# Optimization experiments

Hardware: AMD Instinct MI355X
Metric: run time of the kernel (lower is better)

## Reference

```python
import jax, jax.numpy as jnp
import numpy as np

BN_EPS = 1e-5
NUM_BITS = 8          # activation quantization bits
NUM_BITS_WEIGHT = 8   # weight quantization bits


def _ste(x, q):
    # straight-through estimator: forward = q, backward = identity
    return x + jax.lax.stop_gradient(q - x)


def quant_signed(x, bits):
    # symmetric signed per-tensor uniform quantization (input_signed=True / weights with sign=True)
    qmax = float(2 ** (bits - 1) - 1)
    scale = jnp.max(jnp.abs(x)) / qmax + 1e-12
    q = jnp.clip(jnp.round(x / scale), -qmax - 1.0, qmax) * scale
    return _ste(x, q)


def quant_unsigned(x, bits):
    # unsigned per-tensor uniform quantization (input_signed=False, post-ReLU activations)
    qmax = float(2 ** bits - 1)
    scale = jnp.max(x) / qmax + 1e-12
    q = jnp.clip(jnp.round(x / scale), 0.0, qmax) * scale
    return _ste(x, q)


def conv3x3(x, w, stride=1):
    # x: [N,C,H,W], w: [O,I,3,3], padding=1, no bias
    return jax.lax.conv_general_dilated(
        x, w, window_strides=(stride, stride), padding=((1, 1), (1, 1)),
        dimension_numbers=('NCHW', 'OIHW', 'NCHW'))


def batchnorm(x, gamma, beta):
    # training-mode BN: per-batch statistics over (N,H,W)
    mean = jnp.mean(x, axis=(0, 2, 3), keepdims=True)
    var = jnp.var(x, axis=(0, 2, 3), keepdims=True)
    xn = (x - mean) * jax.lax.rsqrt(var + BN_EPS)
    return xn * gamma[None, :, None, None] + beta[None, :, None, None]


def setup_inputs() -> dict:
    key = jax.random.key(0)
    k1, k2, k3 = jax.random.split(key, 3)
    B, C, H, W = 64, 256, 32, 32
    x = jax.random.normal(k1, (B, C, H, W), dtype=jnp.float32)
    fan = C * 9
    w1 = jax.random.normal(k2, (C, C, 3, 3), dtype=jnp.float32) * np.sqrt(2.0 / fan)
    w2 = jax.random.normal(k3, (C, C, 3, 3), dtype=jnp.float32) * np.sqrt(2.0 / fan)
    gamma1 = jnp.ones((C,), jnp.float32)
    beta1 = jnp.zeros((C,), jnp.float32)
    gamma2 = jnp.ones((C,), jnp.float32)
    beta2 = jnp.zeros((C,), jnp.float32)
    return {'x': x, 'w1': w1, 'gamma1': gamma1, 'beta1': beta1,
            'w2': w2, 'gamma2': gamma2, 'beta2': beta2}


def reference(x, w1, gamma1, beta1, w2, gamma2, beta2):
    residual = x
    # conv1: input_signed=True -> signed 8-bit act quant; weight 8-bit signed quant
    qx = quant_signed(x, NUM_BITS)
    qw1 = quant_signed(w1, NUM_BITS_WEIGHT)
    out = conv3x3(qx, qw1, stride=1)
    out = batchnorm(out, gamma1, beta1)
    out = jax.nn.relu(out)
    # conv2: input_signed=False -> unsigned 8-bit act quant (post-ReLU)
    qo = quant_unsigned(out, NUM_BITS)
    qw2 = quant_signed(w2, NUM_BITS_WEIGHT)
    out = conv3x3(qo, qw2, stride=1)
    out = batchnorm(out, gamma2, beta2)
    out = out + residual
    out = jax.nn.relu(out)
    return out
```

## Files before the change

kernel.cpp:

```cpp
#include <hip/hip_runtime.h>

typedef __attribute__((ext_vector_type(4))) int i32x4;

typedef __attribute__((address_space(1))) unsigned int uglobal;
typedef __attribute__((address_space(3))) unsigned int ulocal;

__device__ __forceinline__ void async16(const void* g, void* l) {
  __builtin_amdgcn_global_load_lds((const uglobal*)g, (ulocal*)l, 16, 0, 0);
}
__device__ __forceinline__ float u2f(unsigned u) { return __uint_as_float(u); }

__global__ __launch_bounds__(256) void absmax3_kernel(const float* __restrict__ x,
                                                      const float* __restrict__ w1,
                                                      const float* __restrict__ w2,
                                                      unsigned* __restrict__ sc) {
  int b = blockIdx.x;
  const float* src; int n4, b0, nb, seg;
  if (b < 1792)      { src = x;  n4 = 4194304; b0 = 0;    nb = 1792; seg = 0; }
  else if (b < 1856) { src = w1; n4 = 147456;  b0 = 1792; nb = 64;   seg = 1; }
  else               { src = w2; n4 = 147456;  b0 = 1856; nb = 64;   seg = 2; }
  float m = 0.f;
  int stride = nb * 256;
  for (int i = (b - b0) * 256 + threadIdx.x; i < n4; i += stride) {
    float4 v = ((const float4*)src)[i];
    m = fmaxf(fmaxf(fabsf(v.x), fabsf(v.y)), fmaxf(fmaxf(fabsf(v.z), fabsf(v.w)), m));
  }
  for (int off = 32; off; off >>= 1) m = fmaxf(m, __shfl_down(m, off, 64));
  __shared__ float sm[4];
  int lane = threadIdx.x & 63, wv = threadIdx.x >> 6;
  if (!lane) sm[wv] = m;
  __syncthreads();
  if (threadIdx.x == 0)
    atomicMax(sc + seg, __float_as_uint(fmaxf(fmaxf(sm[0], sm[1]), fmaxf(sm[2], sm[3]))));
}

__global__ __launch_bounds__(256) void quantw_kernel(const float* __restrict__ w1,
                                                     const float* __restrict__ w2,
                                                     signed char* __restrict__ wq1,
                                                     signed char* __restrict__ wq2,
                                                     const unsigned* __restrict__ sc,
                                                     int* __restrict__ csumT) {
  int b = blockIdx.x, which = b >> 8, o = b & 255, t = threadIdx.x;
  const float* w = which ? w2 : w1;
  signed char* wq = which ? wq2 : wq1;
  float s = u2f(sc[1 + which]) / 127.f + 1e-12f;
  __shared__ float lw[2304];
  for (int j = t; j < 2304; j += 256) lw[j] = w[(size_t)o * 2304 + j];
  __syncthreads();
  int ssum = 0;
#pragma unroll
  for (int tap = 0; tap < 9; ++tap) {
    float q = fminf(fmaxf(rintf(lw[t * 9 + tap] / s), -128.f), 127.f);
    wq[(size_t)o * 2304 + tap * 256 + t] = (signed char)q;
    ssum += (int)q;
  }
  if (which) {
    for (int off = 32; off; off >>= 1) ssum += __shfl_down(ssum, off, 64);
    __shared__ int si[4];
    if (!(t & 63)) si[t >> 6] = ssum;
    __syncthreads();
    if (t == 0) csumT[o] = 128 * (si[0] + si[1] + si[2] + si[3]);
  }
}

__global__ __launch_bounds__(256) void border_kernel(signed char* __restrict__ halo, int v) {
  int n = blockIdx.x;
  int4 val = make_int4(v, v, v, v);
  for (int it = 0; it < 9; ++it) {
    int slot = it * 256 + threadIdx.x;
    if (slot >= 2112) break;
    int cell = slot >> 4, sub = slot & 15;
    int h, w;
    if (cell < 34)      { h = 0;  w = cell; }
    else if (cell < 68) { h = 33; w = cell - 34; }
    else { int j = cell - 68; h = 1 + (j >> 1); w = (j & 1) * 33; }
    *(int4*)(halo + ((size_t)((n * 34 + h) * 34) + w) * 256 + sub * 16) = val;
  }
}

__global__ __launch_bounds__(256) void quantx_kernel(const float* __restrict__ x,
                                                     signed char* __restrict__ halo,
                                                     const unsigned* __restrict__ sc) {
  int n = blockIdx.x >> 5, h = blockIdx.x & 31;
  float s = u2f(sc[0]) / 127.f + 1e-12f;
  __shared__ float lds[32 * 257];
  const float* src = x + (size_t)n * 262144 + h * 32;
  int t = threadIdx.x;
  int wloc = t & 31, crow = t >> 5;
  for (int cc = 0; cc < 256; cc += 8) {
    int c = cc + crow;
    lds[wloc * 257 + c] = src[(size_t)c * 1024 + wloc];
  }
  __syncthreads();
  signed char* dst = halo + ((size_t)((n * 34 + h + 1) * 34) + 1) * 256;
  int c4 = (t & 63) * 4, wsub = t >> 6;
  for (int j = 0; j < 8; ++j) {
    int w_ = wsub * 8 + j;
    char4 q;
    q.x = (signed char)fminf(fmaxf(rintf(lds[w_ * 257 + c4 + 0] / s), -128.f), 127.f);
    q.y = (signed char)fminf(fmaxf(rintf(lds[w_ * 257 + c4 + 1] / s), -128.f), 127.f);
    q.z = (signed char)fminf(fmaxf(rintf(lds[w_ * 257 + c4 + 2] / s), -128.f), 127.f);
    q.w = (signed char)fminf(fmaxf(rintf(lds[w_ * 257 + c4 + 3] / s), -128.f), 127.f);
    *(char4*)(dst + (size_t)w_ * 256 + c4) = q;
  }
}

template <int MODE>
__global__ __launch_bounds__(512) void conv_i8_kernel(const signed char* __restrict__ aptr,
                                                      const signed char* __restrict__ bptr,
                                                      float* __restrict__ out,
                                                      const unsigned* __restrict__ sc,
                                                      float* __restrict__ part,
                                                      const int* __restrict__ csumT) {
  extern __shared__ char smem[];
  const int tid = threadIdx.x, lane = tid & 63, wid = tid >> 6;
  const int wm = wid >> 2, wn = wid & 3;
  int bid = blockIdx.x;
  bid = (bid & 7) * 32 + (bid >> 3);
  const int pixBase = bid * 256;

  long gA[2], gB[2];
  int ldst[2];
#pragma unroll
  for (int j = 0; j < 2; ++j) {
    int d = tid * 16 + j * 8192;
    int rp = d >> 7, s5 = (d >> 4) & 7, sp = s5 ^ (rp & 7);
    int row = rp * 2 + (sp >> 2), kc = (sp & 3) * 16;
    ldst[j] = d;
    int p = pixBase + row;
    int n = p >> 10, h = (p >> 5) & 31, w_ = p & 31;
    long ghalo = (long)((n * 34 + h) * 34 + w_) * 256 + kc;
    long gwt = (long)row * 2304 + kc;
    gA[j] = (MODE == 0) ? ghalo : gwt;
    gB[j] = (MODE == 0) ? gwt : ghalo;
  }

  const int g = lane >> 4, l15 = lane & 15;
  int aOff[8], bOff[4];
#pragma unroll
  for (int m = 0; m < 8; ++m) {
    int row = wm * 128 + m * 16 + l15; int rp = row >> 1;
    aOff[m] = rp * 128 + (((((row & 1) << 2) | g) ^ (rp & 7)) << 4);
  }
#pragma unroll
  for (int n = 0; n < 4; ++n) {
    int row = wn * 64 + n * 16 + l15; int rp = row >> 1;
    bOff[n] = rp * 128 + (((((row & 1) << 2) | g) ^ (rp & 7)) << 4);
  }

  const char* ac = (const char*)aptr;
  const char* bc = (const char*)bptr;
  char* lds = smem;

  auto stageH = [&](int P, int h) {
    int cblk = P / 9, tap = P - cblk * 9;
    int kh = tap / 3, kw = tap - kh * 3;
    long uH = (long)(kh * 34 + kw) * 256 + cblk * 64;
    long uW = (long)tap * 256 + cblk * 64;
    char* rb = lds + (P & 3) * 32768;
    if (h == 0) {
      long uA = (MODE == 0) ? uH : uW;
      async16(ac + gA[0] + uA, rb + ldst[0]);
      async16(ac + gA[1] + uA, rb + ldst[1]);
    } else {
      long uB = (MODE == 0) ? uW : uH;
      async16(bc + gB[0] + uB, rb + 16384 + ldst[0]);
      async16(bc + gB[1] + uB, rb + 16384 + ldst[1]);
    }
  };

  i32x4 acc[8][4];
#pragma unroll
  for (int m = 0; m < 8; ++m)
#pragma unroll
    for (int n = 0; n < 4; ++n)
#pragma unroll
      for (int r = 0; r < 4; ++r) acc[m][n][r] = 0;

  stageH(0, 0); stageH(0, 1); stageH(1, 0); stageH(1, 1); stageH(2, 0); stageH(2, 1);
  asm volatile("s_waitcnt vmcnt(8)" ::: "memory");
  __builtin_amdgcn_s_barrier();

  for (int P = 0; P < 36; ++P) {
    const char* rb = lds + (P & 3) * 32768;
    i32x4 a[8], b[4];
#pragma unroll
    for (int m = 0; m < 4; ++m) a[m] = *(const i32x4*)(rb + aOff[m]);
#pragma unroll
    for (int n = 0; n < 4; ++n) b[n] = *(const i32x4*)(rb + 16384 + bOff[n]);
    if (P < 33) stageH(P + 3, 0);
    __builtin_amdgcn_s_barrier();
    asm volatile("s_waitcnt lgkmcnt(0)" ::: "memory");
    __builtin_amdgcn_sched_barrier(0);
    __builtin_amdgcn_s_setprio(1);
#pragma unroll
    for (int m = 0; m < 4; ++m)
#pragma unroll
      for (int n = 0; n < 4; ++n)
        acc[m][n] = __builtin_amdgcn_mfma_i32_16x16x64_i8(a[m], b[n], acc[m][n], 0, 0, 0);
    __builtin_amdgcn_s_setprio(0);
    __builtin_amdgcn_s_barrier();
#pragma unroll
    for (int m = 4; m < 8; ++m) a[m] = *(const i32x4*)(rb + aOff[m]);
    if (P < 33) stageH(P + 3, 1);
    __builtin_amdgcn_s_barrier();
    asm volatile("s_waitcnt lgkmcnt(0)" ::: "memory");
    __builtin_amdgcn_sched_barrier(0);
    __builtin_amdgcn_s_setprio(1);
#pragma unroll
    for (int m = 4; m < 8; ++m)
#pragma unroll
      for (int n = 0; n < 4; ++n)
        acc[m][n] = __builtin_amdgcn_mfma_i32_16x16x64_i8(a[m], b[n], acc[m][n], 0, 0, 0);
    __builtin_amdgcn_s_setprio(0);
    if (P < 33)       asm volatile("s_waitcnt vmcnt(8)" ::: "memory");
    else if (P == 33) asm volatile("s_waitcnt vmcnt(4)" ::: "memory");
    else if (P == 34) asm volatile("s_waitcnt vmcnt(0)" ::: "memory");
    if (P < 35) __builtin_amdgcn_s_barrier();
  }
  __syncthreads();

  float* twr = (float*)(smem + wid * 17408);

  if constexpr (MODE == 0) {
    const float s = (u2f(sc[0]) / 127.f + 1e-12f) * (u2f(sc[1]) / 127.f + 1e-12f);
    float vs[4], vss[4], vmx[4], vmn[4];
#pragma unroll
    for (int n = 0; n < 4; ++n) { vs[n] = 0.f; vss[n] = 0.f; vmx[n] = -3.4e38f; vmn[n] = 3.4e38f; }
#pragma unroll
    for (int half = 0; half < 2; ++half) {
#pragma unroll
      for (int m2 = 0; m2 < 4; ++m2) {
        int m = half * 4 + m2;
#pragma unroll
        for (int n = 0; n < 4; ++n)
#pragma unroll
          for (int r = 0; r < 4; ++r) {
            float v = (float)acc[m][n][r] * s;
            vs[n] += v; vss[n] += v * v;
            vmx[n] = fmaxf(vmx[n], v); vmn[n] = fminf(vmn[n], v);
            twr[(m2 * 16 + g * 4 + r) * 68 + n * 16 + l15] = v;
          }
      }
#pragma unroll
      for (int it = 0; it < 16; ++it) {
        int i = it * 64 + lane;
        int row = i >> 4, c4 = (i & 15) << 2;
        float4 v4 = *(const float4*)(twr + row * 68 + c4);
        int p = pixBase + wm * 128 + half * 64 + row;
        *(float4*)(out + (size_t)p * 256 + wn * 64 + c4) = v4;
      }
    }
#pragma unroll
    for (int off = 16; off <= 32; off <<= 1)
#pragma unroll
      for (int n = 0; n < 4; ++n) {
        vs[n] += __shfl_xor(vs[n], off, 64);
        vss[n] += __shfl_xor(vss[n], off, 64);
        vmx[n] = fmaxf(vmx[n], __shfl_xor(vmx[n], off, 64));
        vmn[n] = fminf(vmn[n], __shfl_xor(vmn[n], off, 64));
      }
    __syncthreads();
    float* S0 = (float*)(smem + 139264);
    float* S1 = S0 + 512; float* S2 = S0 + 1024; float* S3 = S0 + 1536;
    if (lane < 16) {
#pragma unroll
      for (int n = 0; n < 4; ++n) {
        int ch = wn * 64 + n * 16 + l15;
        S0[wm * 256 + ch] = vs[n]; S1[wm * 256 + ch] = vss[n];
        S2[wm * 256 + ch] = vmx[n]; S3[wm * 256 + ch] = vmn[n];
      }
    }
    __syncthreads();
    if (tid < 256) {
      int idx = bid * 256 + tid;
      part[idx]          = S0[tid] + S0[256 + tid];
      part[65536 + idx]  = S1[tid] + S1[256 + tid];
      part[131072 + idx] = fmaxf(S2[tid], S2[256 + tid]);
      part[196608 + idx] = fminf(S3[tid], S3[256 + tid]);
    }
  } else {
    const float s = (u2f(sc[3]) / 255.f + 1e-12f) * (u2f(sc[2]) / 127.f + 1e-12f);
    float* SS = (float*)(smem + 139264);
    float* SQ = SS + 1024;
#pragma unroll
    for (int half = 0; half < 2; ++half) {
#pragma unroll
      for (int m2 = 0; m2 < 4; ++m2) {
        int m = half * 4 + m2;
        int o0 = wm * 128 + half * 64 + m2 * 16 + g * 4;
        i32x4 tc = *(const i32x4*)(csumT + o0);
        float sr[4] = {0.f, 0.f, 0.f, 0.f}, sq[4] = {0.f, 0.f, 0.f, 0.f};
#pragma unroll
        for (int n = 0; n < 4; ++n)
#pragma unroll
          for (int r = 0; r < 4; ++r) {
            float v = (float)(acc[m][n][r] + tc[r]) * s;
            sr[r] += v; sq[r] += v * v;
            twr[(m2 * 16 + g * 4 + r) * 68 + n * 16 + l15] = v;
          }
#pragma unroll
        for (int off = 1; off <= 8; off <<= 1)
#pragma unroll
          for (int r = 0; r < 4; ++r) {
            sr[r] += __shfl_xor(sr[r], off, 64);
            sq[r] += __shfl_xor(sq[r], off, 64);
          }
        if (l15 == 0) {
#pragma unroll
          for (int r = 0; r < 4; ++r) {
            SS[wn * 256 + o0 + r] = sr[r];
            SQ[wn * 256 + o0 + r] = sq[r];
          }
        }
      }
#pragma unroll
      for (int it = 0; it < 16; ++it) {
        int i = it * 64 + lane;
        int row = i >> 4, c4 = (i & 15) << 2;
        float4 v4 = *(const float4*)(twr + row * 68 + c4);
        int o = wm * 128 + half * 64 + row;
        *(float4*)(out + (size_t)o * 65536 + pixBase + wn * 64 + c4) = v4;
      }
    }
    __syncthreads();
    if (tid < 256) {
      float a = 0.f, b = 0.f;
#pragma unroll
      for (int w = 0; w < 4; ++w) { a += SS[w * 256 + tid]; b += SQ[w * 256 + tid]; }
      part[bid * 256 + tid] = a;
      part[65536 + bid * 256 + tid] = b;
    }
  }
}

__global__ __launch_bounds__(256) void bn1fin_kernel(const float* __restrict__ part,
                                                     const float* __restrict__ g,
                                                     const float* __restrict__ be,
                                                     float* __restrict__ bnA, float* __restrict__ bnB,
                                                     unsigned* __restrict__ sc) {
  int o0 = blockIdx.x * 32;
  int t = threadIdx.x, oc = t & 31, mq = t >> 5;
  float s = 0.f, ss = 0.f, mx = -3.4e38f, mn = 3.4e38f;
  for (int j = 0; j < 32; ++j) {
    int i = (mq * 32 + j) * 256 + o0 + oc;
    s += part[i]; ss += part[65536 + i];
    mx = fmaxf(mx, part[131072 + i]); mn = fminf(mn, part[196608 + i]);
  }
  __shared__ float red[4][8][32];
  red[0][mq][oc] = s; red[1][mq][oc] = ss; red[2][mq][oc] = mx; red[3][mq][oc] = mn;
  __syncthreads();
  if (t < 32) {
    s = 0.f; ss = 0.f; mx = -3.4e38f; mn = 3.4e38f;
    for (int q = 0; q < 8; ++q) {
      s += red[0][q][t]; ss += red[1][q][t];
      mx = fmaxf(mx, red[2][q][t]); mn = fminf(mn, red[3][q][t]);
    }
    float mean = s * (1.f / 65536.f);
    float var = fmaxf(ss * (1.f / 65536.f) - mean * mean, 0.f);
    int o = o0 + t;
    float a = g[o] * rsqrtf(var + 1e-5f);
    float b2 = be[o] - mean * a;
    bnA[o] = a; bnB[o] = b2;
    float m = fmaxf(fmaxf(a * mx + b2, a * mn + b2), 0.f);
    atomicMax(sc + 3, __float_as_uint(m));
  }
}

__global__ __launch_bounds__(256) void bn2fin_kernel(const float* __restrict__ part,
                                                     const float* __restrict__ g,
                                                     const float* __restrict__ be,
                                                     float* __restrict__ bnA2, float* __restrict__ bnB2) {
  int o0 = blockIdx.x * 32;
  int t = threadIdx.x, oc = t & 31, mq = t >> 5;
  float s = 0.f, ss = 0.f;
  for (int j = 0; j < 32; ++j) {
    int i = (mq * 32 + j) * 256 + o0 + oc;
    s += part[i]; ss += part[65536 + i];
  }
  __shared__ float red[2][8][32];
  red[0][mq][oc] = s; red[1][mq][oc] = ss;
  __syncthreads();
  if (t < 32) {
    s = 0.f; ss = 0.f;
    for (int q = 0; q < 8; ++q) { s += red[0][q][t]; ss += red[1][q][t]; }
    float mean = s * (1.f / 65536.f);
    float var = fmaxf(ss * (1.f / 65536.f) - mean * mean, 0.f);
    int o = o0 + t;
    float a = g[o] * rsqrtf(var + 1e-5f);
    bnA2[o] = a;
    bnB2[o] = be[o] - mean * a;
  }
}

__global__ __launch_bounds__(256) void apply_kernel(const float* __restrict__ y,
                                                    const float* __restrict__ bnA,
                                                    const float* __restrict__ bnB,
                                                    const unsigned* __restrict__ sc,
                                                    signed char* __restrict__ halo) {
  int t = threadIdx.x;
  int c4 = (t & 63) * 4;
  int psub = t >> 6;
  float s2 = u2f(sc[3]) / 255.f + 1e-12f;
  float4 a = *(const float4*)(bnA + c4);
  float4 b = *(const float4*)(bnB + c4);
  int p0 = blockIdx.x * 16 + psub;
  for (int j = 0; j < 4; ++j) {
    int p = p0 + j * 4;
    float4 v = *(const float4*)(y + (size_t)p * 256 + c4);
    char4 q;
    q.x = (signed char)((int)fminf(fmaxf(rintf(fmaxf(a.x * v.x + b.x, 0.f) / s2), 0.f), 255.f) - 128);
    q.y = (signed char)((int)fminf(fmaxf(rintf(fmaxf(a.y * v.y + b.y, 0.f) / s2), 0.f), 255.f) - 128);
    q.z = (signed char)((int)fminf(fmaxf(rintf(fmaxf(a.z * v.z + b.z, 0.f) / s2), 0.f), 255.f) - 128);
    q.w = (signed char)((int)fminf(fmaxf(rintf(fmaxf(a.w * v.w + b.w, 0.f) / s2), 0.f), 255.f) - 128);
    int n = p >> 10, h = (p >> 5) & 31, w_ = p & 31;
    *(char4*)(halo + ((size_t)((n * 34 + h + 1) * 34) + (w_ + 1)) * 256 + c4) = q;
  }
}

__global__ __launch_bounds__(256) void final_kernel(const float* __restrict__ y2,
                                                    const float* __restrict__ x,
                                                    const float* __restrict__ bnA2,
                                                    const float* __restrict__ bnB2,
                                                    float* __restrict__ out) {
  int tid = blockIdx.x * 256 + threadIdx.x;
  for (int i = tid; i < 4194304; i += 1048576) {
    int e = i << 2;
    int o = (e >> 10) & 255;
    int n = e >> 18, hw = e & 1023;
    float4 v = *(const float4*)(y2 + (((size_t)o << 16) + (n << 10) + hw));
    float4 xr = ((const float4*)x)[i];
    float a = bnA2[o], b = bnB2[o];
    float4 r;
    r.x = fmaxf(a * v.x + b + xr.x, 0.f);
    r.y = fmaxf(a * v.y + b + xr.y, 0.f);
    r.z = fmaxf(a * v.z + b + xr.z, 0.f);
    r.w = fmaxf(a * v.w + b + xr.w, 0.f);
    ((float4*)out)[i] = r;
  }
}

extern "C" void kernel_launch(void* const* d_in, const int* in_sizes, int n_in,
                              void* d_out, int out_size, void* d_ws, size_t ws_size,
                              hipStream_t stream) {
  const float* x  = (const float*)d_in[0];
  const float* w1 = (const float*)d_in[1];
  const float* g1 = (const float*)d_in[2];
  const float* b1 = (const float*)d_in[3];
  const float* w2 = (const float*)d_in[4];
  const float* g2 = (const float*)d_in[5];
  const float* b2 = (const float*)d_in[6];
  float* out = (float*)d_out;
  char* ws = (char*)d_ws;

  unsigned* sc = (unsigned*)ws;
  float* bnA   = (float*)(ws + 4096);
  float* bnB   = (float*)(ws + 8192);
  float* bnA2  = (float*)(ws + 12288);
  float* bnB2  = (float*)(ws + 16384);
  int*   csumT = (int*)(ws + 20480);
  float* part  = (float*)(ws + 24576);
  signed char* wq1  = (signed char*)(ws + 24576 + 1048576);
  signed char* wq2  = wq1 + 589824;
  signed char* halo = wq2 + 589824;
  float* convb = (float*)(ws + 24576 + 1048576 + 2 * 589824 + 18939904);

  hipFuncSetAttribute((const void*)(conv_i8_kernel<0>), hipFuncAttributeMaxDynamicSharedMemorySize, 147456);
  hipFuncSetAttribute((const void*)(conv_i8_kernel<1>), hipFuncAttributeMaxDynamicSharedMemorySize, 147456);

  hipMemsetAsync(sc, 0, 64, stream);
  border_kernel<<<64, 256, 0, stream>>>(halo, 0);

  absmax3_kernel<<<1920, 256, 0, stream>>>(x, w1, w2, sc);
  quantw_kernel<<<512, 256, 0, stream>>>(w1, w2, wq1, wq2, sc, csumT);
  quantx_kernel<<<2048, 256, 0, stream>>>(x, halo, sc);
  conv_i8_kernel<0><<<256, 512, 147456, stream>>>(halo, wq1, convb, sc, part, csumT);
  bn1fin_kernel<<<8, 256, 0, stream>>>(part, g1, b1, bnA, bnB, sc);
  border_kernel<<<64, 256, 0, stream>>>(halo, (int)0x80808080u);
  apply_kernel<<<4096, 256, 0, stream>>>(convb, bnA, bnB, sc, halo);
  conv_i8_kernel<1><<<256, 512, 147456, stream>>>(wq2, halo, convb, sc, part, csumT);
  bn2fin_kernel<<<8, 256, 0, stream>>>(part, g2, b2, bnA2, bnB2);
  final_kernel<<<4096, 256, 0, stream>>>(convb, x, bnA2, bnB2, out);
}
```

Measured before the change: 315.8 us.

## Fuse BN stats, finalize and apply into conv epilogues via grid barrier

The BN finalize, apply/quantize and final residual kernels are folded into the conv kernels. Per-channel statistics are combined with global atomics (float add plus order-preserving keys for max/min), followed by a software grid-wide barrier, after which each block applies BN in registers and writes either quantized int8 into a second halo buffer or the final output. This removes the fp32 intermediate conv buffer round-trips and several launches. It also simplifies the main loop to a single barrier stage per step, and it relies on all 256 blocks being co-resident for the spin barrier, which risks deadlock and adds atomic contention.

```diff
diff --git a/kernel.cpp b/kernel.cpp
--- a/kernel.cpp
+++ b/kernel.cpp
@@ -9,6 +9,26 @@
   __builtin_amdgcn_global_load_lds((const uglobal*)g, (ulocal*)l, 16, 0, 0);
 }
 __device__ __forceinline__ float u2f(unsigned u) { return __uint_as_float(u); }
+
+__device__ __forceinline__ unsigned fkey(float f) {
+  unsigned u = __float_as_uint(f);
+  return u ^ (unsigned)(((int)u >> 31) | (int)0x80000000);
+}
+__device__ __forceinline__ float funkey(unsigned k) {
+  unsigned u = (k & 0x80000000u) ? (k ^ 0x80000000u) : ~k;
+  return __uint_as_float(u);
+}
+
+__device__ __forceinline__ void gridbar(unsigned* ctr) {
+  __syncthreads();
+  if (threadIdx.x == 0) {
+    __threadfence();
+    atomicAdd(ctr, 1u);
+    while (atomicAdd(ctr, 0u) < 256u) __builtin_amdgcn_s_sleep(2);
+    __threadfence();
+  }
+  __syncthreads();
+}
 
 __global__ __launch_bounds__(256) void absmax3_kernel(const float* __restrict__ x,
                                                       const float* __restrict__ w1,
@@ -63,8 +83,11 @@
   }
 }
 
-__global__ __launch_bounds__(256) void border_kernel(signed char* __restrict__ halo, int v) {
-  int n = blockIdx.x;
+__global__ __launch_bounds__(256) void border_kernel(signed char* __restrict__ h1,
+                                                     signed char* __restrict__ h2) {
+  int which = blockIdx.x >> 6, n = blockIdx.x & 63;
+  signed char* halo = which ? h2 : h1;
+  int v = which ? (int)0x80808080u : 0;
   int4 val = make_int4(v, v, v, v);
   for (int it = 0; it < 9; ++it) {
     int slot = it * 256 + threadIdx.x;
@@ -108,9 +131,13 @@
 template <int MODE>
 __global__ __launch_bounds__(512) void conv_i8_kernel(const signed char* __restrict__ aptr,
                                                       const signed char* __restrict__ bptr,
-                                                      float* __restrict__ out,
-                                                      const unsigned* __restrict__ sc,
-                                                      float* __restrict__ part,
+                                                      const float* __restrict__ xres,
+                                                      float* __restrict__ outp,
+                                                      signed char* __restrict__ halo2,
+                                                      const float* __restrict__ gam,
+                                                      const float* __restrict__ bet,
+                                                      unsigned* __restrict__ sc,
+                                                      float* __restrict__ red,
                                                       const int* __restrict__ csumT) {
   extern __shared__ char smem[];
   const int tid = threadIdx.x, lane = tid & 63, wid = tid >> 6;
@@ -152,21 +179,18 @@
   const char* bc = (const char*)bptr;
   char* lds = smem;
 
-  auto stageH = [&](int P, int h) {
+  auto stage = [&](int P) {
     int cblk = P / 9, tap = P - cblk * 9;
     int kh = tap / 3, kw = tap - kh * 3;
     long uH = (long)(kh * 34 + kw) * 256 + cblk * 64;
     long uW = (long)tap * 256 + cblk * 64;
+    long uA = (MODE == 0) ? uH : uW;
+    long uB = (MODE == 0) ? uW : uH;
     char* rb = lds + (P & 3) * 32768;
-    if (h == 0) {
-      long uA = (MODE == 0) ? uH : uW;
-      async16(ac + gA[0] + uA, rb + ldst[0]);
-      async16(ac + gA[1] + uA, rb + ldst[1]);
-    } else {
-      long uB = (MODE == 0) ? uW : uH;
-      async16(bc + gB[0] + uB, rb + 16384 + ldst[0]);
-      async16(bc + gB[1] + uB, rb + 16384 + ldst[1]);
-    }
+    async16(ac + gA[0] + uA, rb + ldst[0]);
+    async16(ac + gA[1] + uA, rb + ldst[1]);
+    async16(bc + gB[0] + uB, rb + 16384 + ldst[0]);
+    async16(bc + gB[1] + uB, rb + 16384 + ldst[1]);
   };
 
   i32x4 acc[8][4];
@@ -177,38 +201,21 @@
 #pragma unroll
       for (int r = 0; r < 4; ++r) acc[m][n][r] = 0;
 
-  stageH(0, 0); stageH(0, 1); stageH(1, 0); stageH(1, 1); stageH(2, 0); stageH(2, 1);
+  stage(0); stage(1); stage(2);
   asm volatile("s_waitcnt vmcnt(8)" ::: "memory");
-  __builtin_amdgcn_s_barrier();
+  asm volatile("s_barrier" ::: "memory");
 
   for (int P = 0; P < 36; ++P) {
+    if (P < 33) stage(P + 3);
     const char* rb = lds + (P & 3) * 32768;
     i32x4 a[8], b[4];
 #pragma unroll
-    for (int m = 0; m < 4; ++m) a[m] = *(const i32x4*)(rb + aOff[m]);
+    for (int m = 0; m < 8; ++m) a[m] = *(const i32x4*)(rb + aOff[m]);
 #pragma unroll
     for (int n = 0; n < 4; ++n) b[n] = *(const i32x4*)(rb + 16384 + bOff[n]);
-    if (P < 33) stageH(P + 3, 0);
-    __builtin_amdgcn_s_barrier();
-    asm volatile("s_waitcnt lgkmcnt(0)" ::: "memory");
-    __builtin_amdgcn_sched_barrier(0);
     __builtin_amdgcn_s_setprio(1);
 #pragma unroll
-    for (int m = 0; m < 4; ++m)
-#pragma unroll
-      for (int n = 0; n < 4; ++n)
-        acc[m][n] = __builtin_amdgcn_mfma_i32_16x16x64_i8(a[m], b[n], acc[m][n], 0, 0, 0);
-    __builtin_amdgcn_s_setprio(0);
-    __builtin_amdgcn_s_barrier();
-#pragma unroll
-    for (int m = 4; m < 8; ++m) a[m] = *(const i32x4*)(rb + aOff[m]);
-    if (P < 33) stageH(P + 3, 1);
-    __builtin_amdgcn_s_barrier();
-    asm volatile("s_waitcnt lgkmcnt(0)" ::: "memory");
-    __builtin_amdgcn_sched_barrier(0);
-    __builtin_amdgcn_s_setprio(1);
-#pragma unroll
-    for (int m = 4; m < 8; ++m)
+    for (int m = 0; m < 8; ++m)
 #pragma unroll
       for (int n = 0; n < 4; ++n)
         acc[m][n] = __builtin_amdgcn_mfma_i32_16x16x64_i8(a[m], b[n], acc[m][n], 0, 0, 0);
@@ -216,41 +223,27 @@
     if (P < 33)       asm volatile("s_waitcnt vmcnt(8)" ::: "memory");
     else if (P == 33) asm volatile("s_waitcnt vmcnt(4)" ::: "memory");
     else if (P == 34) asm volatile("s_waitcnt vmcnt(0)" ::: "memory");
-    if (P < 35) __builtin_amdgcn_s_barrier();
-  }
-  __syncthreads();
-
+    if (P < 35) asm volatile("s_barrier" ::: "memory");
+  }
+  __syncthreads();
+
+  unsigned* redu = (unsigned*)red;
   float* twr = (float*)(smem + wid * 17408);
 
   if constexpr (MODE == 0) {
-    const float s = (u2f(sc[0]) / 127.f + 1e-12f) * (u2f(sc[1]) / 127.f + 1e-12f);
     float vs[4], vss[4], vmx[4], vmn[4];
 #pragma unroll
     for (int n = 0; n < 4; ++n) { vs[n] = 0.f; vss[n] = 0.f; vmx[n] = -3.4e38f; vmn[n] = 3.4e38f; }
 #pragma unroll
-    for (int half = 0; half < 2; ++half) {
-#pragma unroll
-      for (int m2 = 0; m2 < 4; ++m2) {
-        int m = half * 4 + m2;
-#pragma unroll
-        for (int n = 0; n < 4; ++n)
-#pragma unroll
-          for (int r = 0; r < 4; ++r) {
-            float v = (float)acc[m][n][r] * s;
-            vs[n] += v; vss[n] += v * v;
-            vmx[n] = fmaxf(vmx[n], v); vmn[n] = fminf(vmn[n], v);
-            twr[(m2 * 16 + g * 4 + r) * 68 + n * 16 + l15] = v;
-          }
-      }
-#pragma unroll
-      for (int it = 0; it < 16; ++it) {
-        int i = it * 64 + lane;
-        int row = i >> 4, c4 = (i & 15) << 2;
-        float4 v4 = *(const float4*)(twr + row * 68 + c4);
-        int p = pixBase + wm * 128 + half * 64 + row;
-        *(float4*)(out + (size_t)p * 256 + wn * 64 + c4) = v4;
-      }
-    }
+    for (int m = 0; m < 8; ++m)
+#pragma unroll
+      for (int n = 0; n < 4; ++n)
+#pragma unroll
+        for (int r = 0; r < 4; ++r) {
+          float v = (float)acc[m][n][r];
+          vs[n] += v; vss[n] += v * v;
+          vmx[n] = fmaxf(vmx[n], v); vmn[n] = fminf(vmn[n], v);
+        }
 #pragma unroll
     for (int off = 16; off <= 32; off <<= 1)
 #pragma unroll
@@ -260,7 +253,6 @@
         vmx[n] = fmaxf(vmx[n], __shfl_xor(vmx[n], off, 64));
         vmn[n] = fminf(vmn[n], __shfl_xor(vmn[n], off, 64));
       }
-    __syncthreads();
     float* S0 = (float*)(smem + 139264);
     float* S1 = S0 + 512; float* S2 = S0 + 1024; float* S3 = S0 + 1536;
     if (lane < 16) {
@@ -273,170 +265,161 @@
     }
     __syncthreads();
     if (tid < 256) {
-      int idx = bid * 256 + tid;
-      part[idx]          = S0[tid] + S0[256 + tid];
-      part[65536 + idx]  = S1[tid] + S1[256 + tid];
-      part[131072 + idx] = fmaxf(S2[tid], S2[256 + tid]);
-      part[196608 + idx] = fminf(S3[tid], S3[256 + tid]);
+      atomicAdd(red + tid, S0[tid] + S0[256 + tid]);
+      atomicAdd(red + 256 + tid, S1[tid] + S1[256 + tid]);
+      atomicMax(redu + 512 + tid, fkey(fmaxf(S2[tid], S2[256 + tid])));
+      atomicMin(redu + 768 + tid, fkey(fminf(S3[tid], S3[256 + tid])));
+    }
+    gridbar(sc + 8);
+    float* bnAl = (float*)(smem + 139264);
+    float* bnBl = bnAl + 256;
+    float* rmx  = bnAl + 512;
+    const float sDq = (u2f(sc[0]) / 127.f + 1e-12f) * (u2f(sc[1]) / 127.f + 1e-12f);
+    if (tid < 256) {
+      float su  = atomicAdd(red + tid, 0.f);
+      float sq  = atomicAdd(red + 256 + tid, 0.f);
+      float mxr = funkey(atomicAdd(redu + 512 + tid, 0u));
+      float mnr = funkey(atomicAdd(redu + 768 + tid, 0u));
+      float mean = sDq * su * (1.f / 65536.f);
+      float e2 = sDq * sDq * sq * (1.f / 65536.f);
+      float var = fmaxf(e2 - mean * mean, 0.f);
+      float a = gam[tid] * rsqrtf(var + 1e-5f);
+      float b = bet[tid] - mean * a;
+      float aS = a * sDq;
+      bnAl[tid] = aS; bnBl[tid] = b;
+      rmx[tid] = fmaxf(fmaxf(aS * mxr + b, aS * mnr + b), 0.f);
+    }
+    __syncthreads();
+    for (int st = 128; st; st >>= 1) {
+      if (tid < st) rmx[tid] = fmaxf(rmx[tid], rmx[tid + st]);
+      __syncthreads();
+    }
+    float s2 = rmx[0] * (1.f / 255.f) + 1e-12f;
+    if (tid == 0) ((float*)sc)[3] = s2;
+    float is2 = 1.f / s2;
+    float aCh[4], bCh[4];
+#pragma unroll
+    for (int n = 0; n < 4; ++n) {
+      aCh[n] = bnAl[wn * 64 + n * 16 + l15];
+      bCh[n] = bnBl[wn * 64 + n * 16 + l15];
+    }
+#pragma unroll
+    for (int half = 0; half < 2; ++half) {
+#pragma unroll
+      for (int m2 = 0; m2 < 4; ++m2) {
+        int m = half * 4 + m2;
+#pragma unroll
+        for (int n = 0; n < 4; ++n)
+#pragma unroll
+          for (int r = 0; r < 4; ++r) {
+            float y = fmaxf(aCh[n] * (float)acc[m][n][r] + bCh[n], 0.f);
+            twr[(m2 * 16 + g * 4 + r) * 68 + n * 16 + l15] = y;
+          }
+      }
+#pragma unroll
+      for (int it = 0; it < 16; ++it) {
+        int i = it * 64 + lane;
+        int row = i >> 4, c4 = (i & 15) << 2;
+        float4 y4 = *(const float4*)(twr + row * 68 + c4);
+        char4 q;
+        q.x = (signed char)((int)fminf(fmaxf(rintf(y4.x * is2), 0.f), 255.f) - 128);
+        q.y = (signed char)((int)fminf(fmaxf(rintf(y4.y * is2), 0.f), 255.f) - 128);
+        q.z = (signed char)((int)fminf(fmaxf(rintf(y4.z * is2), 0.f), 255.f) - 128);
+        q.w = (signed char)((int)fminf(fmaxf(rintf(y4.w * is2), 0.f), 255.f) - 128);
+        int p = pixBase + wm * 128 + half * 64 + row;
+        int n_ = p >> 10, h = (p >> 5) & 31, w_ = p & 31;
+        *(char4*)(halo2 + ((size_t)((n_ * 34 + h + 1) * 34) + (w_ + 1)) * 256 + wn * 64 + c4) = q;
+      }
     }
   } else {
-    const float s = (u2f(sc[3]) / 255.f + 1e-12f) * (u2f(sc[2]) / 127.f + 1e-12f);
+    const float s2f = ((const float*)sc)[3];
+    const float sDq = s2f * (u2f(sc[2]) / 127.f + 1e-12f);
     float* SS = (float*)(smem + 139264);
     float* SQ = SS + 1024;
 #pragma unroll
-    for (int half = 0; half < 2; ++half) {
+    for (int half = 0; half < 2; ++half)
 #pragma unroll
       for (int m2 = 0; m2 < 4; ++m2) {
         int m = half * 4 + m2;
         int o0 = wm * 128 + half * 64 + m2 * 16 + g * 4;
         i32x4 tc = *(const i32x4*)(csumT + o0);
-        float sr[4] = {0.f, 0.f, 0.f, 0.f}, sq[4] = {0.f, 0.f, 0.f, 0.f};
+        float sr[4] = {0.f, 0.f, 0.f, 0.f}, sq_[4] = {0.f, 0.f, 0.f, 0.f};
 #pragma unroll
         for (int n = 0; n < 4; ++n)
 #pragma unroll
           for (int r = 0; r < 4; ++r) {
-            float v = (float)(acc[m][n][r] + tc[r]) * s;
-            sr[r] += v; sq[r] += v * v;
-            twr[(m2 * 16 + g * 4 + r) * 68 + n * 16 + l15] = v;
+            float vd = (float)(acc[m][n][r] + tc[r]);
+            sr[r] += vd; sq_[r] += vd * vd;
           }
 #pragma unroll
         for (int off = 1; off <= 8; off <<= 1)
 #pragma unroll
           for (int r = 0; r < 4; ++r) {
             sr[r] += __shfl_xor(sr[r], off, 64);
-            sq[r] += __shfl_xor(sq[r], off, 64);
+            sq_[r] += __shfl_xor(sq_[r], off, 64);
           }
         if (l15 == 0) {
 #pragma unroll
           for (int r = 0; r < 4; ++r) {
             SS[wn * 256 + o0 + r] = sr[r];
-            SQ[wn * 256 + o0 + r] = sq[r];
+            SQ[wn * 256 + o0 + r] = sq_[r];
           }
         }
+      }
+    __syncthreads();
+    if (tid < 256) {
+      float a_ = 0.f, b_ = 0.f;
+#pragma unroll
+      for (int w = 0; w < 4; ++w) { a_ += SS[w * 256 + tid]; b_ += SQ[w * 256 + tid]; }
+      atomicAdd(red + 1024 + tid, a_);
+      atomicAdd(red + 1280 + tid, b_);
+    }
+    gridbar(sc + 9);
+    float* a2l = (float*)(smem + 139264);
+    float* b2l = a2l + 256;
+    if (tid < 256) {
+      float su = atomicAdd(red + 1024 + tid, 0.f);
+      float sq = atomicAdd(red + 1280 + tid, 0.f);
+      float mean = sDq * su * (1.f / 65536.f);
+      float e2 = sDq * sDq * sq * (1.f / 65536.f);
+      float var = fmaxf(e2 - mean * mean, 0.f);
+      float a = gam[tid] * rsqrtf(var + 1e-5f);
+      b2l[tid] = bet[tid] - mean * a;
+      a2l[tid] = a * sDq;
+    }
+    __syncthreads();
+#pragma unroll
+    for (int half = 0; half < 2; ++half) {
+#pragma unroll
+      for (int m2 = 0; m2 < 4; ++m2) {
+        int m = half * 4 + m2;
+        int o0 = wm * 128 + half * 64 + m2 * 16 + g * 4;
+        i32x4 tc = *(const i32x4*)(csumT + o0);
+#pragma unroll
+        for (int n = 0; n < 4; ++n)
+#pragma unroll
+          for (int r = 0; r < 4; ++r)
+            twr[(m2 * 16 + g * 4 + r) * 68 + n * 16 + l15] = (float)(acc[m][n][r] + tc[r]);
       }
 #pragma unroll
       for (int it = 0; it < 16; ++it) {
         int i = it * 64 + lane;
         int row = i >> 4, c4 = (i & 15) << 2;
+        int o = wm * 128 + half * 64 + row;
         float4 v4 = *(const float4*)(twr + row * 68 + c4);
-        int o = wm * 128 + half * 64 + row;
-        *(float4*)(out + (size_t)o * 65536 + pixBase + wn * 64 + c4) = v4;
-      }
-    }
-    __syncthreads();
-    if (tid < 256) {
-      float a = 0.f, b = 0.f;
-#pragma unroll
-      for (int w = 0; w < 4; ++w) { a += SS[w * 256 + tid]; b += SQ[w * 256 + tid]; }
-      part[bid * 256 + tid] = a;
-      part[65536 + bid * 256 + tid] = b;
-    }
-  }
-}
-
-__global__ __launch_bounds__(256) void bn1fin_kernel(const float* __restrict__ part,
-                                                     const float* __restrict__ g,
-                                                     const float* __restrict__ be,
-                                                     float* __restrict__ bnA, float* __restrict__ bnB,
-                                                     unsigned* __restrict__ sc) {
-  int o0 = blockIdx.x * 32;
-  int t = threadIdx.x, oc = t & 31, mq = t >> 5;
-  float s = 0.f, ss = 0.f, mx = -3.4e38f, mn = 3.4e38f;
-  for (int j = 0; j < 32; ++j) {
-    int i = (mq * 32 + j) * 256 + o0 + oc;
-    s += part[i]; ss += part[65536 + i];
-    mx = fmaxf(mx, part[131072 + i]); mn = fminf(mn, part[196608 + i]);
-  }
-  __shared__ float red[4][8][32];
-  red[0][mq][oc] = s; red[1][mq][oc] = ss; red[2][mq][oc] = mx; red[3][mq][oc] = mn;
-  __syncthreads();
-  if (t < 32) {
-    s = 0.f; ss = 0.f; mx = -3.4e38f; mn = 3.4e38f;
-    for (int q = 0; q < 8; ++q) {
-      s += red[0][q][t]; ss += red[1][q][t];
-      mx = fmaxf(mx, red[2][q][t]); mn = fminf(mn, red[3][q][t]);
-    }
-    float mean = s * (1.f / 65536.f);
-    float var = fmaxf(ss * (1.f / 65536.f) - mean * mean, 0.f);
-    int o = o0 + t;
-    float a = g[o] * rsqrtf(var + 1e-5f);
-    float b2 = be[o] - mean * a;
-    bnA[o] = a; bnB[o] = b2;
-    float m = fmaxf(fmaxf(a * mx + b2, a * mn + b2), 0.f);
-    atomicMax(sc + 3, __float_as_uint(m));
-  }
-}
-
-__global__ __launch_bounds__(256) void bn2fin_kernel(const float* __restrict__ part,
-                                                     const float* __restrict__ g,
-                                                     const float* __restrict__ be,
-                                                     float* __restrict__ bnA2, float* __restrict__ bnB2) {
-  int o0 = blockIdx.x * 32;
-  int t = threadIdx.x, oc = t & 31, mq = t >> 5;
-  float s = 0.f, ss = 0.f;
-  for (int j = 0; j < 32; ++j) {
-    int i = (mq * 32 + j) * 256 + o0 + oc;
-    s += part[i]; ss += part[65536 + i];
-  }
-  __shared__ float red[2][8][32];
-  red[0][mq][oc] = s; red[1][mq][oc] = ss;
-  __syncthreads();
-  if (t < 32) {
-    s = 0.f; ss = 0.f;
-    for (int q = 0; q < 8; ++q) { s += red[0][q][t]; ss += red[1][q][t]; }
-    float mean = s * (1.f / 65536.f);
-    float var = fmaxf(ss * (1.f / 65536.f) - mean * mean, 0.f);
-    int o = o0 + t;
-    float a = g[o] * rsqrtf(var + 1e-5f);
-    bnA2[o] = a;
-    bnB2[o] = be[o] - mean * a;
-  }
-}
-
-__global__ __launch_bounds__(256) void apply_kernel(const float* __restrict__ y,
-                                                    const float* __restrict__ bnA,
-                                                    const float* __restrict__ bnB,
-                                                    const unsigned* __restrict__ sc,
-                                                    signed char* __restrict__ halo) {
-  int t = threadIdx.x;
-  int c4 = (t & 63) * 4;
-  int psub = t >> 6;
-  float s2 = u2f(sc[3]) / 255.f + 1e-12f;
-  float4 a = *(const float4*)(bnA + c4);
-  float4 b = *(const float4*)(bnB + c4);
-  int p0 = blockIdx.x * 16 + psub;
-  for (int j = 0; j < 4; ++j) {
-    int p = p0 + j * 4;
-    float4 v = *(const float4*)(y + (size_t)p * 256 + c4);
-    char4 q;
-    q.x = (signed char)((int)fminf(fmaxf(rintf(fmaxf(a.x * v.x + b.x, 0.f) / s2), 0.f), 255.f) - 128);
-    q.y = (signed char)((int)fminf(fmaxf(rintf(fmaxf(a.y * v.y + b.y, 0.f) / s2), 0.f), 255.f) - 128);
-    q.z = (signed char)((int)fminf(fmaxf(rintf(fmaxf(a.z * v.z + b.z, 0.f) / s2), 0.f), 255.f) - 128);
-    q.w = (signed char)((int)fminf(fmaxf(rintf(fmaxf(a.w * v.w + b.w, 0.f) / s2), 0.f), 255.f) - 128);
-    int n = p >> 10, h = (p >> 5) & 31, w_ = p & 31;
-    *(char4*)(halo + ((size_t)((n * 34 + h + 1) * 34) + (w_ + 1)) * 256 + c4) = q;
-  }
-}
-
-__global__ __launch_bounds__(256) void final_kernel(const float* __restrict__ y2,
-                                                    const float* __restrict__ x,
-                                                    const float* __restrict__ bnA2,
-                                                    const float* __restrict__ bnB2,
-                                                    float* __restrict__ out) {
-  int tid = blockIdx.x * 256 + threadIdx.x;
-  for (int i = tid; i < 4194304; i += 1048576) {
-    int e = i << 2;
-    int o = (e >> 10) & 255;
-    int n = e >> 18, hw = e & 1023;
-    float4 v = *(const float4*)(y2 + (((size_t)o << 16) + (n << 10) + hw));
-    float4 xr = ((const float4*)x)[i];
-    float a = bnA2[o], b = bnB2[o];
-    float4 r;
-    r.x = fmaxf(a * v.x + b + xr.x, 0.f);
-    r.y = fmaxf(a * v.y + b + xr.y, 0.f);
-    r.z = fmaxf(a * v.z + b + xr.z, 0.f);
-    r.w = fmaxf(a * v.w + b + xr.w, 0.f);
-    ((float4*)out)[i] = r;
+        int p = pixBase + wn * 64 + c4;
+        int n_ = p >> 10, hw = p & 1023;
+        size_t base = ((size_t)n_ << 18) + ((size_t)o << 10) + hw;
+        float4 x4 = *(const float4*)(xres + base);
+        float a = a2l[o], b = b2l[o];
+        float4 r4;
+        r4.x = fmaxf(a * v4.x + b + x4.x, 0.f);
+        r4.y = fmaxf(a * v4.y + b + x4.y, 0.f);
+        r4.z = fmaxf(a * v4.z + b + x4.z, 0.f);
+        r4.w = fmaxf(a * v4.w + b + x4.w, 0.f);
+        *(float4*)(outp + base) = r4;
+      }
+    }
   }
 }
 
@@ -454,31 +437,26 @@
   char* ws = (char*)d_ws;
 
   unsigned* sc = (unsigned*)ws;
-  float* bnA   = (float*)(ws + 4096);
-  float* bnB   = (float*)(ws + 8192);
-  float* bnA2  = (float*)(ws + 12288);
-  float* bnB2  = (float*)(ws + 16384);
-  int*   csumT = (int*)(ws + 20480);
-  float* part  = (float*)(ws + 24576);
-  signed char* wq1  = (signed char*)(ws + 24576 + 1048576);
-  signed char* wq2  = wq1 + 589824;
-  signed char* halo = wq2 + 589824;
-  float* convb = (float*)(ws + 24576 + 1048576 + 2 * 589824 + 18939904);
+  float* red   = (float*)(ws + 1024);
+  int* csumT   = (int*)(ws + 7168);
+  signed char* wq1   = (signed char*)(ws + 8192);
+  signed char* wq2   = wq1 + 589824;
+  signed char* halo1 = wq2 + 589824;
+  signed char* halo2 = halo1 + 18939904;
 
   hipFuncSetAttribute((const void*)(conv_i8_kernel<0>), hipFuncAttributeMaxDynamicSharedMemorySize, 147456);
   hipFuncSetAttribute((const void*)(conv_i8_kernel<1>), hipFuncAttributeMaxDynamicSharedMemorySize, 147456);
 
-  hipMemsetAsync(sc, 0, 64, stream);
-  border_kernel<<<64, 256, 0, stream>>>(halo, 0);
-
+  hipMemsetAsync(ws, 0, 4096, stream);
+  hipMemsetAsync(ws + 4096, 0xFF, 1024, stream);
+  hipMemsetAsync(ws + 5120, 0, 2048, stream);
+
+  border_kernel<<<128, 256, 0, stream>>>(halo1, halo2);
   absmax3_kernel<<<1920, 256, 0, stream>>>(x, w1, w2, sc);
   quantw_kernel<<<512, 256, 0, stream>>>(w1, w2, wq1, wq2, sc, csumT);
-  quantx_kernel<<<2048, 256, 0, stream>>>(x, halo, sc);
-  conv_i8_kernel<0><<<256, 512, 147456, stream>>>(halo, wq1, convb, sc, part, csumT);
-  bn1fin_kernel<<<8, 256, 0, stream>>>(part, g1, b1, bnA, bnB, sc);
-  border_kernel<<<64, 256, 0, stream>>>(halo, (int)0x80808080u);
-  apply_kernel<<<4096, 256, 0, stream>>>(convb, bnA, bnB, sc, halo);
-  conv_i8_kernel<1><<<256, 512, 147456, stream>>>(wq2, halo, convb, sc, part, csumT);
-  bn2fin_kernel<<<8, 256, 0, stream>>>(part, g2, b2, bnA2, bnB2);
-  final_kernel<<<4096, 256, 0, stream>>>(convb, x, bnA2, bnB2, out);
-}
+  quantx_kernel<<<2048, 256, 0, stream>>>(x, halo1, sc);
+  conv_i8_kernel<0><<<256, 512, 147456, stream>>>(halo1, wq1, nullptr, nullptr, halo2,
+                                                  g1, b1, sc, red, csumT);
+  conv_i8_kernel<1><<<256, 512, 147456, stream>>>(wq2, halo2, x, out, nullptr,
+                                                  g2, b2, sc, red, csumT);
+}
```

After: 301.1 us. 1.05x faster.
